# Kernel optimization log

Hardware: AMD Instinct MI355X
Metric: run time of the kernel (lower is better)

Reference implementation:

```python
import jax, jax.numpy as jnp
import numpy as np

LOG2 = float(np.log(2.0))

def ssp(x):
    # shifted softplus: softplus(x) - log(2)
    return jax.nn.softplus(x) - LOG2

N_NODES = 50000
N_EDGES = 600000
HID = 128
NF = 128

def setup_inputs() -> dict:
    key = jax.random.key(0)
    ks = jax.random.split(key, 10)
    x = jax.random.normal(ks[0], (N_NODES, HID), dtype=jnp.float32)
    edge_attr = jax.random.normal(ks[1], (N_EDGES, NF), dtype=jnp.float32)
    edge_index = jax.random.randint(ks[2], (2, N_EDGES), 0, N_NODES, dtype=jnp.int32)
    s = 1.0 / np.sqrt(NF)
    fc1_w = jax.random.uniform(ks[3], (NF, HID), jnp.float32, -s, s)   # CFConv.fc1 (no bias)
    f_w1 = jax.random.uniform(ks[4], (NF, NF), jnp.float32, -s, s)     # filter_mlp[0]
    f_b1 = jnp.zeros((NF,), jnp.float32)
    f_w2 = jax.random.uniform(ks[5], (NF, NF), jnp.float32, -s, s)     # filter_mlp[2]
    f_b2 = jnp.zeros((NF,), jnp.float32)
    s_w1 = jax.random.uniform(ks[6], (NF, NF), jnp.float32, -s, s)     # StateMLP.fc1
    s_w2 = jax.random.uniform(ks[7], (NF, NF), jnp.float32, -s, s)     # StateMLP.fc2
    return {"x": x, "edge_attr": edge_attr, "edge_index": edge_index,
            "fc1_w": fc1_w, "f_w1": f_w1, "f_b1": f_b1, "f_w2": f_w2,
            "f_b2": f_b2, "s_w1": s_w1, "s_w2": s_w2}

def reference(x, edge_attr, edge_index, fc1_w, f_w1, f_b1, f_w2, f_b2, s_w1, s_w2):
    src, dst = edge_index[0], edge_index[1]  # x_j = x[src], aggregate at dst
    # filter network on edge attributes: [E, NF]
    W = ssp(ssp(edge_attr @ f_w1.T + f_b1) @ f_w2.T + f_b2)
    # message: gather source nodes, linear transform, filter multiply
    msg = (x[src] @ fc1_w.T) * W                               # [E, NF]
    # scatter-add aggregation into nodes
    agg = jax.ops.segment_sum(msg, dst, num_segments=x.shape[0])  # [N, NF]
    # StateMLP
    return ssp(agg @ s_w1.T) @ s_w2.T
```

## Files before the change

### kernel.cpp

```cpp
#include <hip/hip_runtime.h>

#define F 128
#define SP 16

typedef __attribute__((ext_vector_type(8))) __bf16 bf16x8;
typedef __attribute__((ext_vector_type(4))) float floatx4;
typedef __attribute__((ext_vector_type(2))) _Float16 f16x2;

__device__ __forceinline__ float ssp(float x) {
    return __logf(fmaf(0.5f, __expf(x), 0.5f));
}

__global__ void prep_kernel(const float* __restrict__ fc1w,
                            const float* __restrict__ fw1,
                            const float* __restrict__ fw2,
                            const float* __restrict__ sw1,
                            const float* __restrict__ sw2,
                            __bf16* __restrict__ fc1h, __bf16* __restrict__ fc1l,
                            __bf16* __restrict__ fw1h, __bf16* __restrict__ fw2h,
                            __bf16* __restrict__ sw1h, __bf16* __restrict__ sw1l,
                            __bf16* __restrict__ sw2h, __bf16* __restrict__ sw2l,
                            int* __restrict__ cnt, int N)
{
    int i = blockIdx.x * blockDim.x + threadIdx.x;
    for (int j = i; j < N; j += gridDim.x * blockDim.x) cnt[j] = 0;
    if (i >= F * F) return;
    float v; __bf16 h;
    v = fc1w[i]; h = (__bf16)v; fc1h[i] = h; fc1l[i] = (__bf16)(v - (float)h);
    v = sw1[i];  h = (__bf16)v; sw1h[i] = h; sw1l[i] = (__bf16)(v - (float)h);
    v = sw2[i];  h = (__bf16)v; sw2h[i] = h; sw2l[i] = (__bf16)(v - (float)h);
    fw1h[i] = (__bf16)fw1[i];
    fw2h[i] = (__bf16)fw2[i];
}

__global__ __launch_bounds__(256) void hist_kernel(const int* __restrict__ eidx,
                                                   int* __restrict__ cnt, int E)
{
    int i = blockIdx.x * 256 + threadIdx.x;
    if (i < E) atomicAdd(&cnt[eidx[E + i]], 1);
}

__global__ __launch_bounds__(1024) void scan1_kernel(int* __restrict__ cnt,
                                                     int* __restrict__ bsums, int N)
{
    __shared__ int sd[1024];
    const int t = threadIdx.x;
    const int i = blockIdx.x * 1024 + t;
    int v = (i < N) ? cnt[i] : 0;
    sd[t] = v;
    __syncthreads();
    for (int off = 1; off < 1024; off <<= 1) {
        int add = (t >= off) ? sd[t - off] : 0;
        __syncthreads();
        sd[t] += add;
        __syncthreads();
    }
    if (i < N) cnt[i] = sd[t] - v;
    if (t == 1023) bsums[blockIdx.x] = sd[t];
}

__global__ void scan2_kernel(int* __restrict__ bsums, int nb)
{
    const int lane = threadIdx.x & 63;
    int v = (lane < nb) ? bsums[lane] : 0;
    int acc = v;
    #pragma unroll
    for (int off = 1; off < 64; off <<= 1) {
        int t = __shfl_up(acc, off);
        if (lane >= off) acc += t;
    }
    if (lane < nb) bsums[lane] = acc - v;
}

__global__ __launch_bounds__(1024) void scan3_kernel(int* __restrict__ cnt,
                                                     const int* __restrict__ bsums, int N)
{
    int i = blockIdx.x * 1024 + threadIdx.x;
    if (i < N) cnt[i] += bsums[blockIdx.x];
}

__global__ __launch_bounds__(256) void scatter_kernel(const int* __restrict__ eidx,
                                                      int* __restrict__ cursor,
                                                      int* __restrict__ pos,
                                                      int* __restrict__ ssrc,
                                                      int* __restrict__ sdst, int E)
{
    int i = blockIdx.x * 256 + threadIdx.x;
    if (i < E) {
        int d = eidx[E + i];
        int slot = atomicAdd(&cursor[d], 1);
        pos[i] = slot;
        ssrc[slot] = eidx[i];
        sdst[slot] = d;
    }
}

__global__ __launch_bounds__(256) void fc1_kernel(
    const float* __restrict__ x, const __bf16* __restrict__ wh,
    const __bf16* __restrict__ wl, float* __restrict__ y, int M)
{
    const int tid = threadIdx.x;
    const int wv = tid >> 6, lane = tid & 63;
    const int m16 = lane & 15, q = lane >> 4;
    const int g = wv & 1, c = wv >> 1;
    const int rowA0 = blockIdx.x * 32 + g * 16 + m16;
    const int rowA = rowA0 < M ? rowA0 : M - 1;

    floatx4 acc[4] = {};
    #pragma unroll
    for (int ks = 0; ks < 4; ++ks) {
        const int kb = ks * 32 + q * 8;
        const float4* p = (const float4*)(x + (size_t)rowA * F + kb);
        float4 a0 = p[0], a1 = p[1];
        float fv[8] = {a0.x, a0.y, a0.z, a0.w, a1.x, a1.y, a1.z, a1.w};
        bf16x8 ah, al;
        #pragma unroll
        for (int i = 0; i < 8; ++i) {
            __bf16 h = (__bf16)fv[i];
            ah[i] = h; al[i] = (__bf16)(fv[i] - (float)h);
        }
        #pragma unroll
        for (int nt = 0; nt < 4; ++nt) {
            const size_t wo = (size_t)(c * 64 + nt * 16 + m16) * F + kb;
            bf16x8 bh = *(const bf16x8*)(wh + wo);
            bf16x8 bl = *(const bf16x8*)(wl + wo);
            acc[nt] = __builtin_amdgcn_mfma_f32_16x16x32_bf16(ah, bh, acc[nt], 0, 0, 0);
            acc[nt] = __builtin_amdgcn_mfma_f32_16x16x32_bf16(al, bh, acc[nt], 0, 0, 0);
            acc[nt] = __builtin_amdgcn_mfma_f32_16x16x32_bf16(ah, bl, acc[nt], 0, 0, 0);
        }
    }
    const int rowD0 = blockIdx.x * 32 + g * 16 + q * 4;
    #pragma unroll
    for (int nt = 0; nt < 4; ++nt) {
        const int col = c * 64 + nt * 16 + m16;
        #pragma unroll
        for (int r = 0; r < 4; ++r) {
            const int row = rowD0 + r;
            if (row < M) y[(size_t)row * F + col] = acc[nt][r];
        }
    }
}

__global__ __launch_bounds__(256) void filter_kernel(
    const float* __restrict__ edge_attr,
    const int* __restrict__ pos,
    const float* __restrict__ fb1, const float* __restrict__ fb2,
    const __bf16* __restrict__ fw1, const __bf16* __restrict__ fw2,
    _Float16* __restrict__ Ws, int E)
{
    __shared__ __align__(16) unsigned short smem[64][136];
    __shared__ int pos_s[64];
    __bf16 (*h1)[136] = (__bf16 (*)[136])smem;
    _Float16 (*wo)[136] = (_Float16 (*)[136])smem;

    const int tid = threadIdx.x;
    const int wv = tid >> 6, lane = tid & 63;
    const int m16 = lane & 15, q = lane >> 4;
    const int e0 = blockIdx.x * 64;
    if (tid < 64) { int e = e0 + tid; pos_s[tid] = pos[e < E ? e : E - 1]; }
    const int rowA0 = e0 + wv * 16 + m16;
    const int rowA = rowA0 < E ? rowA0 : E - 1;

    floatx4 acc[8] = {};
    #pragma unroll
    for (int ks = 0; ks < 4; ++ks) {
        const int kb = ks * 32 + q * 8;
        const float4* pa = (const float4*)(edge_attr + (size_t)rowA * F + kb);
        float4 a0 = pa[0], a1 = pa[1];
        float fv[8] = {a0.x, a0.y, a0.z, a0.w, a1.x, a1.y, a1.z, a1.w};
        bf16x8 aF;
        #pragma unroll
        for (int i = 0; i < 8; ++i) aF[i] = (__bf16)fv[i];
        #pragma unroll
        for (int nt = 0; nt < 8; ++nt) {
            bf16x8 bF = *(const bf16x8*)(fw1 + (size_t)(nt * 16 + m16) * F + kb);
            acc[nt] = __builtin_amdgcn_mfma_f32_16x16x32_bf16(aF, bF, acc[nt], 0, 0, 0);
        }
    }
    #pragma unroll
    for (int nt = 0; nt < 8; ++nt) {
        const int col = nt * 16 + m16;
        const float b = fb1[col];
        #pragma unroll
        for (int r = 0; r < 4; ++r) {
            const int row = wv * 16 + q * 4 + r;
            h1[row][col] = (__bf16)ssp(acc[nt][r] + b);
        }
    }
    __syncthreads();

    floatx4 zero = {};
    #pragma unroll
    for (int nt = 0; nt < 8; ++nt) acc[nt] = zero;
    #pragma unroll
    for (int ks = 0; ks < 4; ++ks) {
        const int kb = ks * 32 + q * 8;
        bf16x8 aF = *(const bf16x8*)(&h1[wv * 16 + m16][kb]);
        #pragma unroll
        for (int nt = 0; nt < 8; ++nt) {
            bf16x8 bF = *(const bf16x8*)(fw2 + (size_t)(nt * 16 + m16) * F + kb);
            acc[nt] = __builtin_amdgcn_mfma_f32_16x16x32_bf16(aF, bF, acc[nt], 0, 0, 0);
        }
    }
    __syncthreads();

    #pragma unroll
    for (int nt = 0; nt < 8; ++nt) {
        const int col = nt * 16 + m16;
        const float b = fb2[col];
        #pragma unroll
        for (int r = 0; r < 4; ++r) {
            const int row = wv * 16 + q * 4 + r;
            wo[row][col] = (_Float16)ssp(acc[nt][r] + b);
        }
    }
    __syncthreads();

    #pragma unroll
    for (int r2 = 0; r2 < 4; ++r2) {
        const int row = wv * 16 + r2 * 4 + q;
        const int e = e0 + row;
        if (e < E) {
            const uint4 v = *(const uint4*)(&wo[row][m16 * 8]);
            *(uint4*)(Ws + (size_t)pos_s[row] * F + m16 * 8) = v;
        }
    }
}

__global__ __launch_bounds__(256) void agg_kernel(
    const float* __restrict__ y, const _Float16* __restrict__ Ws,
    const int* __restrict__ ssrc, const int* __restrict__ sdst,
    float* __restrict__ agg, int E)
{
    const int tid = threadIdx.x;
    const int wv = tid >> 6, lane = tid & 63;
    const long s0 = ((long)blockIdx.x * 4 + wv) * SP;
    if (s0 >= E) return;

    int msrc = 0, mdst = -1;
    if (lane < SP) {
        long s = s0 + lane;
        if (s < E) { msrc = ssrc[s]; mdst = sdst[s]; }
    }
    const int col = lane * 2;
    float rx = 0.f, ry = 0.f;
    int rdst = -1;

    #pragma unroll
    for (int c = 0; c < SP / 4; ++c) {
        float2 yv[4]; float wx[4], wy[4]; int pdst[4]; bool okr[4];
        #pragma unroll
        for (int r = 0; r < 4; ++r) {
            const int p = c * 4 + r;
            const long s = s0 + p;
            okr[r] = (s < E);
            const int sp = __shfl(msrc, p);
            pdst[r] = __shfl(mdst, p);
            const long sc = okr[r] ? s : (long)(E - 1);
            const int spc = okr[r] ? sp : 0;
            yv[r] = *(const float2*)(y + (size_t)spc * F + col);
            f16x2 w2 = *(const f16x2*)(Ws + (size_t)sc * F + col);
            wx[r] = (float)w2[0]; wy[r] = (float)w2[1];
        }
        #pragma unroll
        for (int r = 0; r < 4; ++r) {
            if (!okr[r]) continue;
            if (pdst[r] != rdst) {
                if (rdst >= 0) {
                    unsafeAtomicAdd(&agg[(size_t)rdst * F + col], rx);
                    unsafeAtomicAdd(&agg[(size_t)rdst * F + col + 1], ry);
                }
                rx = 0.f; ry = 0.f; rdst = pdst[r];
            }
            rx = fmaf(yv[r].x, wx[r], rx);
            ry = fmaf(yv[r].y, wy[r], ry);
        }
    }
    if (rdst >= 0) {
        unsafeAtomicAdd(&agg[(size_t)rdst * F + col], rx);
        unsafeAtomicAdd(&agg[(size_t)rdst * F + col + 1], ry);
    }
}

__global__ __launch_bounds__(256) void state_kernel(
    const float* __restrict__ agg,
    const __bf16* __restrict__ w1h, const __bf16* __restrict__ w1l,
    const __bf16* __restrict__ w2h, const __bf16* __restrict__ w2l,
    float* __restrict__ out, int M)
{
    __shared__ __bf16 hh[32][136];
    __shared__ __bf16 hl[32][136];

    const int tid = threadIdx.x;
    const int wv = tid >> 6, lane = tid & 63;
    const int m16 = lane & 15, q = lane >> 4;
    const int g = wv & 1, c = wv >> 1;
    const int rowA0 = blockIdx.x * 32 + g * 16 + m16;
    const int rowA = rowA0 < M ? rowA0 : M - 1;

    floatx4 acc[4] = {};
    #pragma unroll
    for (int ks = 0; ks < 4; ++ks) {
        const int kb = ks * 32 + q * 8;
        const float4* p = (const float4*)(agg + (size_t)rowA * F + kb);
        float4 a0 = p[0], a1 = p[1];
        float fv[8] = {a0.x, a0.y, a0.z, a0.w, a1.x, a1.y, a1.z, a1.w};
        bf16x8 ah, al;
        #pragma unroll
        for (int i = 0; i < 8; ++i) {
            __bf16 h = (__bf16)fv[i];
            ah[i] = h; al[i] = (__bf16)(fv[i] - (float)h);
        }
        #pragma unroll
        for (int nt = 0; nt < 4; ++nt) {
            const size_t wo = (size_t)(c * 64 + nt * 16 + m16) * F + kb;
            bf16x8 bh = *(const bf16x8*)(w1h + wo);
            bf16x8 bl = *(const bf16x8*)(w1l + wo);
            acc[nt] = __builtin_amdgcn_mfma_f32_16x16x32_bf16(ah, bh, acc[nt], 0, 0, 0);
            acc[nt] = __builtin_amdgcn_mfma_f32_16x16x32_bf16(al, bh, acc[nt], 0, 0, 0);
            acc[nt] = __builtin_amdgcn_mfma_f32_16x16x32_bf16(ah, bl, acc[nt], 0, 0, 0);
        }
    }
    #pragma unroll
    for (int nt = 0; nt < 4; ++nt) {
        const int col = c * 64 + nt * 16 + m16;
        #pragma unroll
        for (int r = 0; r < 4; ++r) {
            const int row = g * 16 + q * 4 + r;
            const float h = ssp(acc[nt][r]);
            const __bf16 H = (__bf16)h;
            hh[row][col] = H;
            hl[row][col] = (__bf16)(h - (float)H);
        }
    }
    __syncthreads();

    floatx4 zero = {};
    #pragma unroll
    for (int nt = 0; nt < 4; ++nt) acc[nt] = zero;
    #pragma unroll
    for (int ks = 0; ks < 4; ++ks) {
        const int kb = ks * 32 + q * 8;
        bf16x8 aH = *(const bf16x8*)(&hh[g * 16 + m16][kb]);
        bf16x8 aL = *(const bf16x8*)(&hl[g * 16 + m16][kb]);
        #pragma unroll
        for (int nt = 0; nt < 4; ++nt) {
            const size_t wo = (size_t)(c * 64 + nt * 16 + m16) * F + kb;
            bf16x8 bh = *(const bf16x8*)(w2h + wo);
            bf16x8 bl = *(const bf16x8*)(w2l + wo);
            acc[nt] = __builtin_amdgcn_mfma_f32_16x16x32_bf16(aH, bh, acc[nt], 0, 0, 0);
            acc[nt] = __builtin_amdgcn_mfma_f32_16x16x32_bf16(aL, bh, acc[nt], 0, 0, 0);
            acc[nt] = __builtin_amdgcn_mfma_f32_16x16x32_bf16(aH, bl, acc[nt], 0, 0, 0);
        }
    }
    const int rowD0 = blockIdx.x * 32 + g * 16 + q * 4;
    #pragma unroll
    for (int nt = 0; nt < 4; ++nt) {
        const int col = c * 64 + nt * 16 + m16;
        #pragma unroll
        for (int r = 0; r < 4; ++r) {
            const int row = rowD0 + r;
            if (row < M) out[(size_t)row * F + col] = acc[nt][r];
        }
    }
}

extern "C" void kernel_launch(void* const* d_in, const int* in_sizes, int n_in,
                              void* d_out, int out_size, void* d_ws, size_t ws_size,
                              hipStream_t stream)
{
    const float* x         = (const float*)d_in[0];
    const float* edge_attr = (const float*)d_in[1];
    const int*   eidx      = (const int*)d_in[2];
    const float* fc1w      = (const float*)d_in[3];
    const float* fw1       = (const float*)d_in[4];
    const float* fb1       = (const float*)d_in[5];
    const float* fw2       = (const float*)d_in[6];
    const float* fb2       = (const float*)d_in[7];
    const float* sw1       = (const float*)d_in[8];
    const float* sw2       = (const float*)d_in[9];
    float* out = (float*)d_out;

    const int N = in_sizes[0] / F;
    const int E = in_sizes[1] / F;

    float* agg = (float*)d_ws;
    float* y   = agg + (size_t)N * F;
    __bf16* wb = (__bf16*)(y + (size_t)N * F);
    const int WSZ = F * F;
    __bf16* fc1h = wb;            __bf16* fc1l = wb + WSZ;
    __bf16* fw1h = wb + 2 * WSZ;  __bf16* fw2h = wb + 3 * WSZ;
    __bf16* sw1h = wb + 4 * WSZ;  __bf16* sw1l = wb + 5 * WSZ;
    __bf16* sw2h = wb + 6 * WSZ;  __bf16* sw2l = wb + 7 * WSZ;
    _Float16* Ws = (_Float16*)(wb + 8 * WSZ);
    int* cnt   = (int*)(Ws + (size_t)E * F);
    int* bsums = cnt + N;
    int* pos   = bsums + 64;
    int* ssrc  = pos + E;
    int* sdst  = ssrc + E;

    const int nb1 = (N + 1023) / 1024;

    hipMemsetAsync(agg, 0, (size_t)N * F * sizeof(float), stream);

    prep_kernel<<<(WSZ + 255) / 256, 256, 0, stream>>>(
        fc1w, fw1, fw2, sw1, sw2, fc1h, fc1l, fw1h, fw2h, sw1h, sw1l, sw2h, sw2l,
        cnt, N);

    fc1_kernel<<<(N + 31) / 32, 256, 0, stream>>>(x, fc1h, fc1l, y, N);

    hist_kernel<<<(E + 255) / 256, 256, 0, stream>>>(eidx, cnt, E);
    scan1_kernel<<<nb1, 1024, 0, stream>>>(cnt, bsums, N);
    scan2_kernel<<<1, 64, 0, stream>>>(bsums, nb1);
    scan3_kernel<<<nb1, 1024, 0, stream>>>(cnt, bsums, N);
    scatter_kernel<<<(E + 255) / 256, 256, 0, stream>>>(eidx, cnt, pos, ssrc, sdst, E);

    filter_kernel<<<(E + 63) / 64, 256, 0, stream>>>(
        edge_attr, pos, fb1, fb2, fw1h, fw2h, Ws, E);

    agg_kernel<<<(E + 63) / 64, 256, 0, stream>>>(y, Ws, ssrc, sdst, agg, E);

    state_kernel<<<(N + 31) / 32, 256, 0, stream>>>(
        agg, sw1h, sw1l, sw2h, sw2l, out, N);
}
```

Measured before the change: 966.4 us.

## Retile dense GEMM kernels so each wave owns full output rows

The fc1 and state kernels now give each wave a 16-row strip with all 128 output columns, so a block covers 64 rows instead of 32. The filter kernel now gives each wave 32 edges, two 16-row MFMA tiles that share each weight-fragment load, with per-wave shared buffers. Weight fragments are loaded into register arrays before the MFMA chains, and launch bounds request 3 blocks per SM. The aim is better reuse of weight loads per MFMA and more independent MFMA chains, at the cost of higher register pressure and fewer blocks.

```diff
diff --git a/kernel.cpp b/kernel.cpp
--- a/kernel.cpp
+++ b/kernel.cpp
@@ -9,6 +9,10 @@
 
 __device__ __forceinline__ float ssp(float x) {
     return __logf(fmaf(0.5f, __expf(x), 0.5f));
+}
+
+__device__ __forceinline__ floatx4 mfma_bf16(bf16x8 a, bf16x8 b, floatx4 c) {
+    return __builtin_amdgcn_mfma_f32_16x16x32_bf16(a, b, c, 0, 0, 0);
 }
 
 __global__ void prep_kernel(const float* __restrict__ fc1w,
@@ -95,18 +99,18 @@
     }
 }
 
-__global__ __launch_bounds__(256) void fc1_kernel(
+__global__ __launch_bounds__(256, 3) void fc1_kernel(
     const float* __restrict__ x, const __bf16* __restrict__ wh,
     const __bf16* __restrict__ wl, float* __restrict__ y, int M)
 {
     const int tid = threadIdx.x;
     const int wv = tid >> 6, lane = tid & 63;
     const int m16 = lane & 15, q = lane >> 4;
-    const int g = wv & 1, c = wv >> 1;
-    const int rowA0 = blockIdx.x * 32 + g * 16 + m16;
+    const int r0 = blockIdx.x * 64 + wv * 16;
+    const int rowA0 = r0 + m16;
     const int rowA = rowA0 < M ? rowA0 : M - 1;
 
-    floatx4 acc[4] = {};
+    floatx4 acc[8] = {};
     #pragma unroll
     for (int ks = 0; ks < 4; ++ks) {
         const int kb = ks * 32 + q * 8;
@@ -119,62 +123,77 @@
             __bf16 h = (__bf16)fv[i];
             ah[i] = h; al[i] = (__bf16)(fv[i] - (float)h);
         }
-        #pragma unroll
-        for (int nt = 0; nt < 4; ++nt) {
-            const size_t wo = (size_t)(c * 64 + nt * 16 + m16) * F + kb;
-            bf16x8 bh = *(const bf16x8*)(wh + wo);
-            bf16x8 bl = *(const bf16x8*)(wl + wo);
-            acc[nt] = __builtin_amdgcn_mfma_f32_16x16x32_bf16(ah, bh, acc[nt], 0, 0, 0);
-            acc[nt] = __builtin_amdgcn_mfma_f32_16x16x32_bf16(al, bh, acc[nt], 0, 0, 0);
-            acc[nt] = __builtin_amdgcn_mfma_f32_16x16x32_bf16(ah, bl, acc[nt], 0, 0, 0);
-        }
-    }
-    const int rowD0 = blockIdx.x * 32 + g * 16 + q * 4;
-    #pragma unroll
-    for (int nt = 0; nt < 4; ++nt) {
-        const int col = c * 64 + nt * 16 + m16;
-        #pragma unroll
-        for (int r = 0; r < 4; ++r) {
-            const int row = rowD0 + r;
+        bf16x8 bH[8], bL[8];
+        #pragma unroll
+        for (int nt = 0; nt < 8; ++nt) {
+            const size_t wo = (size_t)(nt * 16 + m16) * F + kb;
+            bH[nt] = *(const bf16x8*)(wh + wo);
+            bL[nt] = *(const bf16x8*)(wl + wo);
+        }
+        #pragma unroll
+        for (int nt = 0; nt < 8; ++nt) {
+            acc[nt] = mfma_bf16(ah, bH[nt], acc[nt]);
+            acc[nt] = mfma_bf16(al, bH[nt], acc[nt]);
+            acc[nt] = mfma_bf16(ah, bL[nt], acc[nt]);
+        }
+    }
+    #pragma unroll
+    for (int nt = 0; nt < 8; ++nt) {
+        const int col = nt * 16 + m16;
+        #pragma unroll
+        for (int r = 0; r < 4; ++r) {
+            const int row = r0 + q * 4 + r;
             if (row < M) y[(size_t)row * F + col] = acc[nt][r];
         }
     }
 }
 
-__global__ __launch_bounds__(256) void filter_kernel(
+__global__ __launch_bounds__(256, 3) void filter_kernel(
     const float* __restrict__ edge_attr,
     const int* __restrict__ pos,
     const float* __restrict__ fb1, const float* __restrict__ fb2,
     const __bf16* __restrict__ fw1, const __bf16* __restrict__ fw2,
     _Float16* __restrict__ Ws, int E)
 {
-    __shared__ __align__(16) unsigned short smem[64][136];
-    __shared__ int pos_s[64];
-    __bf16 (*h1)[136] = (__bf16 (*)[136])smem;
-    _Float16 (*wo)[136] = (_Float16 (*)[136])smem;
+    __shared__ __align__(16) unsigned short smem[4][32][136];
+    __shared__ int pos_s[4][32];
 
     const int tid = threadIdx.x;
     const int wv = tid >> 6, lane = tid & 63;
     const int m16 = lane & 15, q = lane >> 4;
-    const int e0 = blockIdx.x * 64;
-    if (tid < 64) { int e = e0 + tid; pos_s[tid] = pos[e < E ? e : E - 1]; }
-    const int rowA0 = e0 + wv * 16 + m16;
-    const int rowA = rowA0 < E ? rowA0 : E - 1;
-
-    floatx4 acc[8] = {};
+    const int e0 = blockIdx.x * 128 + wv * 32;
+
+    __bf16 (*h1)[136] = (__bf16 (*)[136])smem[wv];
+    _Float16 (*wo)[136] = (_Float16 (*)[136])smem[wv];
+
+    if (lane < 32) { int e = e0 + lane; pos_s[wv][lane] = pos[e < E ? e : E - 1]; }
+
+    const int rA0 = e0 + m16;
+    const int rA1 = e0 + 16 + m16;
+    const int r0c = rA0 < E ? rA0 : E - 1;
+    const int r1c = rA1 < E ? rA1 : E - 1;
+
+    floatx4 acc0[8] = {}, acc1[8] = {};
     #pragma unroll
     for (int ks = 0; ks < 4; ++ks) {
         const int kb = ks * 32 + q * 8;
-        const float4* pa = (const float4*)(edge_attr + (size_t)rowA * F + kb);
-        float4 a0 = pa[0], a1 = pa[1];
-        float fv[8] = {a0.x, a0.y, a0.z, a0.w, a1.x, a1.y, a1.z, a1.w};
-        bf16x8 aF;
-        #pragma unroll
-        for (int i = 0; i < 8; ++i) aF[i] = (__bf16)fv[i];
-        #pragma unroll
-        for (int nt = 0; nt < 8; ++nt) {
-            bf16x8 bF = *(const bf16x8*)(fw1 + (size_t)(nt * 16 + m16) * F + kb);
-            acc[nt] = __builtin_amdgcn_mfma_f32_16x16x32_bf16(aF, bF, acc[nt], 0, 0, 0);
+        const float4* p0 = (const float4*)(edge_attr + (size_t)r0c * F + kb);
+        const float4* p1 = (const float4*)(edge_attr + (size_t)r1c * F + kb);
+        float4 a00 = p0[0], a01 = p0[1];
+        float4 a10 = p1[0], a11 = p1[1];
+        float f0[8] = {a00.x, a00.y, a00.z, a00.w, a01.x, a01.y, a01.z, a01.w};
+        float f1[8] = {a10.x, a10.y, a10.z, a10.w, a11.x, a11.y, a11.z, a11.w};
+        bf16x8 aF0, aF1;
+        #pragma unroll
+        for (int i = 0; i < 8; ++i) { aF0[i] = (__bf16)f0[i]; aF1[i] = (__bf16)f1[i]; }
+        bf16x8 bF[8];
+        #pragma unroll
+        for (int nt = 0; nt < 8; ++nt)
+            bF[nt] = *(const bf16x8*)(fw1 + (size_t)(nt * 16 + m16) * F + kb);
+        #pragma unroll
+        for (int nt = 0; nt < 8; ++nt) {
+            acc0[nt] = mfma_bf16(aF0, bF[nt], acc0[nt]);
+            acc1[nt] = mfma_bf16(aF1, bF[nt], acc1[nt]);
         }
     }
     #pragma unroll
@@ -183,23 +202,28 @@
         const float b = fb1[col];
         #pragma unroll
         for (int r = 0; r < 4; ++r) {
-            const int row = wv * 16 + q * 4 + r;
-            h1[row][col] = (__bf16)ssp(acc[nt][r] + b);
+            h1[q * 4 + r][col]      = (__bf16)ssp(acc0[nt][r] + b);
+            h1[16 + q * 4 + r][col] = (__bf16)ssp(acc1[nt][r] + b);
         }
     }
     __syncthreads();
 
     floatx4 zero = {};
     #pragma unroll
-    for (int nt = 0; nt < 8; ++nt) acc[nt] = zero;
+    for (int nt = 0; nt < 8; ++nt) { acc0[nt] = zero; acc1[nt] = zero; }
     #pragma unroll
     for (int ks = 0; ks < 4; ++ks) {
         const int kb = ks * 32 + q * 8;
-        bf16x8 aF = *(const bf16x8*)(&h1[wv * 16 + m16][kb]);
-        #pragma unroll
-        for (int nt = 0; nt < 8; ++nt) {
-            bf16x8 bF = *(const bf16x8*)(fw2 + (size_t)(nt * 16 + m16) * F + kb);
-            acc[nt] = __builtin_amdgcn_mfma_f32_16x16x32_bf16(aF, bF, acc[nt], 0, 0, 0);
+        bf16x8 aF0 = *(const bf16x8*)(&h1[m16][kb]);
+        bf16x8 aF1 = *(const bf16x8*)(&h1[16 + m16][kb]);
+        bf16x8 bF[8];
+        #pragma unroll
+        for (int nt = 0; nt < 8; ++nt)
+            bF[nt] = *(const bf16x8*)(fw2 + (size_t)(nt * 16 + m16) * F + kb);
+        #pragma unroll
+        for (int nt = 0; nt < 8; ++nt) {
+            acc0[nt] = mfma_bf16(aF0, bF[nt], acc0[nt]);
+            acc1[nt] = mfma_bf16(aF1, bF[nt], acc1[nt]);
         }
     }
     __syncthreads();
@@ -210,19 +234,19 @@
         const float b = fb2[col];
         #pragma unroll
         for (int r = 0; r < 4; ++r) {
-            const int row = wv * 16 + q * 4 + r;
-            wo[row][col] = (_Float16)ssp(acc[nt][r] + b);
+            wo[q * 4 + r][col]      = (_Float16)ssp(acc0[nt][r] + b);
+            wo[16 + q * 4 + r][col] = (_Float16)ssp(acc1[nt][r] + b);
         }
     }
     __syncthreads();
 
     #pragma unroll
-    for (int r2 = 0; r2 < 4; ++r2) {
-        const int row = wv * 16 + r2 * 4 + q;
+    for (int it = 0; it < 8; ++it) {
+        const int row = it * 4 + q;
         const int e = e0 + row;
         if (e < E) {
             const uint4 v = *(const uint4*)(&wo[row][m16 * 8]);
-            *(uint4*)(Ws + (size_t)pos_s[row] * F + m16 * 8) = v;
+            *(uint4*)(Ws + (size_t)pos_s[wv][row] * F + m16 * 8) = v;
         }
     }
 }
@@ -282,23 +306,26 @@
     }
 }
 
-__global__ __launch_bounds__(256) void state_kernel(
+__global__ __launch_bounds__(256, 3) void state_kernel(
     const float* __restrict__ agg,
     const __bf16* __restrict__ w1h, const __bf16* __restrict__ w1l,
     const __bf16* __restrict__ w2h, const __bf16* __restrict__ w2l,
     float* __restrict__ out, int M)
 {
-    __shared__ __bf16 hh[32][136];
-    __shared__ __bf16 hl[32][136];
+    __shared__ __align__(16) __bf16 hhs[4][16][136];
+    __shared__ __align__(16) __bf16 hls[4][16][136];
 
     const int tid = threadIdx.x;
     const int wv = tid >> 6, lane = tid & 63;
     const int m16 = lane & 15, q = lane >> 4;
-    const int g = wv & 1, c = wv >> 1;
-    const int rowA0 = blockIdx.x * 32 + g * 16 + m16;
+    const int r0 = blockIdx.x * 64 + wv * 16;
+    const int rowA0 = r0 + m16;
     const int rowA = rowA0 < M ? rowA0 : M - 1;
 
-    floatx4 acc[4] = {};
+    __bf16 (*hh)[136] = hhs[wv];
+    __bf16 (*hl)[136] = hls[wv];
+
+    floatx4 acc[8] = {};
     #pragma unroll
     for (int ks = 0; ks < 4; ++ks) {
         const int kb = ks * 32 + q * 8;
@@ -311,22 +338,26 @@
             __bf16 h = (__bf16)fv[i];
             ah[i] = h; al[i] = (__bf16)(fv[i] - (float)h);
         }
-        #pragma unroll
-        for (int nt = 0; nt < 4; ++nt) {
-            const size_t wo = (size_t)(c * 64 + nt * 16 + m16) * F + kb;
-            bf16x8 bh = *(const bf16x8*)(w1h + wo);
-            bf16x8 bl = *(const bf16x8*)(w1l + wo);
-            acc[nt] = __builtin_amdgcn_mfma_f32_16x16x32_bf16(ah, bh, acc[nt], 0, 0, 0);
-            acc[nt] = __builtin_amdgcn_mfma_f32_16x16x32_bf16(al, bh, acc[nt], 0, 0, 0);
-            acc[nt] = __builtin_amdgcn_mfma_f32_16x16x32_bf16(ah, bl, acc[nt], 0, 0, 0);
-        }
-    }
-    #pragma unroll
-    for (int nt = 0; nt < 4; ++nt) {
-        const int col = c * 64 + nt * 16 + m16;
-        #pragma unroll
-        for (int r = 0; r < 4; ++r) {
-            const int row = g * 16 + q * 4 + r;
+        bf16x8 bH[8], bL[8];
+        #pragma unroll
+        for (int nt = 0; nt < 8; ++nt) {
+            const size_t wo = (size_t)(nt * 16 + m16) * F + kb;
+            bH[nt] = *(const bf16x8*)(w1h + wo);
+            bL[nt] = *(const bf16x8*)(w1l + wo);
+        }
+        #pragma unroll
+        for (int nt = 0; nt < 8; ++nt) {
+            acc[nt] = mfma_bf16(ah, bH[nt], acc[nt]);
+            acc[nt] = mfma_bf16(al, bH[nt], acc[nt]);
+            acc[nt] = mfma_bf16(ah, bL[nt], acc[nt]);
+        }
+    }
+    #pragma unroll
+    for (int nt = 0; nt < 8; ++nt) {
+        const int col = nt * 16 + m16;
+        #pragma unroll
+        for (int r = 0; r < 4; ++r) {
+            const int row = q * 4 + r;
             const float h = ssp(acc[nt][r]);
             const __bf16 H = (__bf16)h;
             hh[row][col] = H;
@@ -337,29 +368,32 @@
 
     floatx4 zero = {};
     #pragma unroll
-    for (int nt = 0; nt < 4; ++nt) acc[nt] = zero;
+    for (int nt = 0; nt < 8; ++nt) acc[nt] = zero;
     #pragma unroll
     for (int ks = 0; ks < 4; ++ks) {
         const int kb = ks * 32 + q * 8;
-        bf16x8 aH = *(const bf16x8*)(&hh[g * 16 + m16][kb]);
-        bf16x8 aL = *(const bf16x8*)(&hl[g * 16 + m16][kb]);
-        #pragma unroll
-        for (int nt = 0; nt < 4; ++nt) {
-            const size_t wo = (size_t)(c * 64 + nt * 16 + m16) * F + kb;
-            bf16x8 bh = *(const bf16x8*)(w2h + wo);
-            bf16x8 bl = *(const bf16x8*)(w2l + wo);
-            acc[nt] = __builtin_amdgcn_mfma_f32_16x16x32_bf16(aH, bh, acc[nt], 0, 0, 0);
-            acc[nt] = __builtin_amdgcn_mfma_f32_16x16x32_bf16(aL, bh, acc[nt], 0, 0, 0);
-            acc[nt] = __builtin_amdgcn_mfma_f32_16x16x32_bf16(aH, bl, acc[nt], 0, 0, 0);
-        }
-    }
-    const int rowD0 = blockIdx.x * 32 + g * 16 + q * 4;
-    #pragma unroll
-    for (int nt = 0; nt < 4; ++nt) {
-        const int col = c * 64 + nt * 16 + m16;
-        #pragma unroll
-        for (int r = 0; r < 4; ++r) {
-            const int row = rowD0 + r;
+        bf16x8 aH = *(const bf16x8*)(&hh[m16][kb]);
+        bf16x8 aL = *(const bf16x8*)(&hl[m16][kb]);
+        bf16x8 bH[8], bL[8];
+        #pragma unroll
+        for (int nt = 0; nt < 8; ++nt) {
+            const size_t wo = (size_t)(nt * 16 + m16) * F + kb;
+            bH[nt] = *(const bf16x8*)(w2h + wo);
+            bL[nt] = *(const bf16x8*)(w2l + wo);
+        }
+        #pragma unroll
+        for (int nt = 0; nt < 8; ++nt) {
+            acc[nt] = mfma_bf16(aH, bH[nt], acc[nt]);
+            acc[nt] = mfma_bf16(aL, bH[nt], acc[nt]);
+            acc[nt] = mfma_bf16(aH, bL[nt], acc[nt]);
+        }
+    }
+    #pragma unroll
+    for (int nt = 0; nt < 8; ++nt) {
+        const int col = nt * 16 + m16;
+        #pragma unroll
+        for (int r = 0; r < 4; ++r) {
+            const int row = r0 + q * 4 + r;
             if (row < M) out[(size_t)row * F + col] = acc[nt][r];
         }
     }
@@ -407,7 +441,7 @@
         fc1w, fw1, fw2, sw1, sw2, fc1h, fc1l, fw1h, fw2h, sw1h, sw1l, sw2h, sw2l,
         cnt, N);
 
-    fc1_kernel<<<(N + 31) / 32, 256, 0, stream>>>(x, fc1h, fc1l, y, N);
+    fc1_kernel<<<(N + 63) / 64, 256, 0, stream>>>(x, fc1h, fc1l, y, N);
 
     hist_kernel<<<(E + 255) / 256, 256, 0, stream>>>(eidx, cnt, E);
     scan1_kernel<<<nb1, 1024, 0, stream>>>(cnt, bsums, N);
@@ -415,11 +449,11 @@
     scan3_kernel<<<nb1, 1024, 0, stream>>>(cnt, bsums, N);
     scatter_kernel<<<(E + 255) / 256, 256, 0, stream>>>(eidx, cnt, pos, ssrc, sdst, E);
 
-    filter_kernel<<<(E + 63) / 64, 256, 0, stream>>>(
+    filter_kernel<<<(E + 127) / 128, 256, 0, stream>>>(
         edge_attr, pos, fb1, fb2, fw1h, fw2h, Ws, E);
 
     agg_kernel<<<(E + 63) / 64, 256, 0, stream>>>(y, Ws, ssrc, sdst, agg, E);
 
-    state_kernel<<<(N + 31) / 32, 256, 0, stream>>>(
+    state_kernel<<<(N + 63) / 64, 256, 0, stream>>>(
         agg, sw1h, sw1l, sw2h, sw2l, out, N);
 }
```

New measurement: 849.2 us. -12.1%, faster.
